# Kernel tuning notes

Hardware: AMD Instinct MI355X
Metric: run time of the kernel (lower is better)

The kernel has to match this reference:

```python
import jax, jax.numpy as jnp
import numpy as np

E, D, O, G, H, K = 8, 1024, 1024, 512, 2048, 2
B = 8192

def _xavier(key, shape):
    fan_in, fan_out = shape[-2], shape[-1]
    lim = float(np.sqrt(6.0 / (fan_in + fan_out)))
    return jax.random.uniform(key, shape, jnp.float32, -lim, lim)

def setup_inputs() -> dict:
    key = jax.random.key(0)
    ks = jax.random.split(key, 6)
    x = jax.random.normal(ks[0], (B, D), jnp.float32)
    # stacked expert params (xavier-uniform weights, zero bias like torch init)
    W1 = _xavier(ks[1], (E, D, H))
    b1 = jnp.zeros((E, H), jnp.float32)
    W2 = _xavier(ks[2], (E, H, O))
    b2 = jnp.zeros((E, O), jnp.float32)
    # gate params
    Wg1 = _xavier(ks[3], (D, G))
    bg1 = jnp.zeros((G,), jnp.float32)
    Wg2 = _xavier(ks[4], (G, E))
    bg2 = jnp.zeros((E,), jnp.float32)
    return {"x": x, "W1": W1, "b1": b1, "W2": W2, "b2": b2,
            "Wg1": Wg1, "bg1": bg1, "Wg2": Wg2, "bg2": bg2}

def reference(x, W1, b1, W2, b2, Wg1, bg1, Wg2, bg2):
    batch = x.shape[0]
    # gate (dropout inactive in eval)
    gate_logits = jax.nn.relu(x @ Wg1 + bg1) @ Wg2 + bg2          # [B,E]
    gate_scores = jax.nn.softmax(gate_logits, axis=1)
    top_k_scores, top_k_indices = jax.lax.top_k(gate_scores, K)   # [B,K]
    # dense all-expert MLP (mirrors torch.stack over experts)
    h = jax.nn.relu(jnp.einsum('bd,edh->ebh', x, W1) + b1[:, None, :])   # [E,B,H]
    expert_outputs = jnp.einsum('ebh,eho->beo', h, W2) + b2[None, :, :]  # [B,E,O]
    # gather top-k expert outputs, scale, combine
    selected = jnp.take_along_axis(expert_outputs, top_k_indices[:, :, None], axis=1)  # [B,K,O]
    scaled = selected * top_k_scores[:, :, None]
    scaled = scaled / (jnp.sum(top_k_scores, axis=1, keepdims=True)[:, :, None] + 1e-9)
    combined = jnp.sum(scaled, axis=1)                            # [B,O]
    # auxiliary loss
    one_hot = jax.nn.one_hot(top_k_indices, E, dtype=jnp.float32) # [B,K,E]
    expert_load = jnp.sum(one_hot, axis=(0, 1)) / (batch + 1e-9)
    load_balancing_loss = jnp.var(expert_load, ddof=1)            # torch var is unbiased
    entropy = -jnp.mean(jnp.sum(gate_scores * jnp.log(gate_scores + 1e-9), axis=1))
    aux_loss = load_balancing_loss + entropy
    return combined, aux_loss
```

## Files before the change

kernel.cpp:

```cpp
#include <hip/hip_runtime.h>

#define B_ 8192
#define D_ 1024
#define O_ 1024
#define G_ 512
#define H_ 2048
#define E_ 8
#define ROWSP (B_ * 2 + E_ * 128)
#define TAU 0.01f

typedef unsigned short u16;
using f32x4 = __attribute__((ext_vector_type(4))) float;
using s16x8 = __attribute__((ext_vector_type(8))) short;

__device__ __forceinline__ u16 f2bf(float f) {
  union { float f; unsigned u; } v; v.f = f;
  unsigned r = v.u + 0x7FFFu + ((v.u >> 16) & 1u);
  return (u16)(r >> 16);
}
__device__ __forceinline__ float bf2f(u16 h) {
  union { unsigned u; float f; } v; v.u = ((unsigned)h) << 16; return v.f;
}
__device__ __forceinline__ void gload16(const void* g, void* l) {
  __builtin_amdgcn_global_load_lds(
      (const __attribute__((address_space(1))) unsigned int*)g,
      (__attribute__((address_space(3))) unsigned int*)l, 16, 0, 0);
}
__device__ __forceinline__ int xcd_swz(int bid, int nwg) {
  return (bid & 7) * (nwg >> 3) + (bid >> 3);
}
__device__ __forceinline__ int stage_kc(int t) {
  return (((t & 3) ^ ((t >> 3) & 3)) * 8);
}
__device__ __forceinline__ int frag_idx(int half, int lane, int i) {
  int row = half * 64 + i * 16 + (lane & 15);
  int s = (lane >> 4) ^ ((lane >> 1) & 3);
  return (row * 4 + s) * 8;
}

#define PREP_CAST_BLK (B_ * D_ / 4 / 256)
#define PREP_WG1_BLK  ((G_ / 32) * (D_ / 32))
#define PREP_W1_BLK   ((H_ / 32) * (D_ / 32) * E_)
#define PREP_W2_BLK   ((O_ / 32) * (H_ / 32) * E_)

__device__ __forceinline__ void tr_cast_tile(const float* __restrict__ src,
                                             u16* __restrict__ dhi,
                                             u16* __restrict__ dlo,
                                             int R, int C, int bx, int by,
                                             float (*tile)[33], int t) {
  int tx = t & 31, ty = t >> 5;
  int c0 = bx * 32, r0 = by * 32;
#pragma unroll
  for (int p = 0; p < 4; ++p) {
    int r = ty + p * 8;
    tile[r][tx] = src[(size_t)(r0 + r) * C + c0 + tx];
  }
  __syncthreads();
#pragma unroll
  for (int p = 0; p < 4; ++p) {
    int r = ty + p * 8;
    float v = tile[tx][r];
    size_t o = (size_t)(c0 + r) * R + r0 + tx;
    dhi[o] = f2bf(v);
    if (dlo) dlo[o] = f2bf(v - bf2f(f2bf(v)));
  }
}

__global__ __launch_bounds__(256) void k_prep(const float* __restrict__ x,
                                              u16* __restrict__ xhi, u16* __restrict__ xlo,
                                              const float* __restrict__ Wg1,
                                              u16* __restrict__ wg1h, u16* __restrict__ wg1l,
                                              const float* __restrict__ W1, u16* __restrict__ w1t,
                                              const float* __restrict__ W2, u16* __restrict__ w2t) {
  __shared__ float tile[32][33];
  int t = threadIdx.x;
  int b = blockIdx.x;
  if (b < PREP_CAST_BLK) {
    int i = b * 256 + t;
    float4 v = ((const float4*)x)[i];
    u16 h0 = f2bf(v.x), h1 = f2bf(v.y), h2 = f2bf(v.z), h3 = f2bf(v.w);
    ushort4 hi; hi.x = h0; hi.y = h1; hi.z = h2; hi.w = h3;
    ushort4 lo;
    lo.x = f2bf(v.x - bf2f(h0)); lo.y = f2bf(v.y - bf2f(h1));
    lo.z = f2bf(v.z - bf2f(h2)); lo.w = f2bf(v.w - bf2f(h3));
    ((ushort4*)xhi)[i] = hi; ((ushort4*)xlo)[i] = lo;
    return;
  }
  b -= PREP_CAST_BLK;
  if (b < PREP_WG1_BLK) {
    tr_cast_tile(Wg1, wg1h, wg1l, D_, G_, b & 15, b >> 4, tile, t);
    return;
  }
  b -= PREP_WG1_BLK;
  if (b < PREP_W1_BLK) {
    int e = b >> 11, rr = b & 2047;
    size_t ofs = (size_t)e * D_ * H_;
    tr_cast_tile(W1 + ofs, w1t + ofs, nullptr, D_, H_, rr & 63, rr >> 6, tile, t);
    return;
  }
  b -= PREP_W1_BLK;
  {
    int e = b >> 11, rr = b & 2047;
    size_t ofs = (size_t)e * H_ * O_;
    tr_cast_tile(W2 + ofs, w2t + ofs, nullptr, H_, O_, rr & 31, rr >> 5, tile, t);
  }
}

__global__ __launch_bounds__(256) void k_gate_gemm1(const u16* __restrict__ xhi,
                                                    const u16* __restrict__ xlo,
                                                    const u16* __restrict__ whi,
                                                    const u16* __restrict__ wlo,
                                                    const float* __restrict__ bg1,
                                                    float* __restrict__ G1) {
  __shared__ u16 Ah[4096], Al[4096], Bh[4096], Bl[4096];
  int work = xcd_swz(blockIdx.x, (G_ / 128) * (B_ / 128));
  int m0 = (work >> 2) * 128, n0 = (work & 3) * 128;
  int t = threadIdx.x;
  int wave = t >> 6, lane = t & 63;
  int wm = wave >> 1, wn = wave & 1;

  const f32x4 z = {0.f, 0.f, 0.f, 0.f};
  f32x4 acc[4][4];
#pragma unroll
  for (int i = 0; i < 4; ++i)
#pragma unroll
    for (int j = 0; j < 4; ++j) acc[i][j] = z;

  int ar = t >> 2, ac = stage_kc(t);
  const u16* xh0 = xhi + (size_t)(m0 + ar) * D_ + ac;
  const u16* xh1 = xhi + (size_t)(m0 + 64 + ar) * D_ + ac;
  const u16* xl0 = xlo + (size_t)(m0 + ar) * D_ + ac;
  const u16* xl1 = xlo + (size_t)(m0 + 64 + ar) * D_ + ac;
  const u16* wh0 = whi + (size_t)(n0 + ar) * D_ + ac;
  const u16* wh1 = whi + (size_t)(n0 + 64 + ar) * D_ + ac;
  const u16* wl0 = wlo + (size_t)(n0 + ar) * D_ + ac;
  const u16* wl1 = wlo + (size_t)(n0 + 64 + ar) * D_ + ac;

  for (int k0 = 0; k0 < D_; k0 += 32) {
    gload16(xh0 + k0, &Ah[t * 8]); gload16(xh1 + k0, &Ah[2048 + t * 8]);
    gload16(xl0 + k0, &Al[t * 8]); gload16(xl1 + k0, &Al[2048 + t * 8]);
    gload16(wh0 + k0, &Bh[t * 8]); gload16(wh1 + k0, &Bh[2048 + t * 8]);
    gload16(wl0 + k0, &Bl[t * 8]); gload16(wl1 + k0, &Bl[2048 + t * 8]);
    __syncthreads();
    s16x8 ah[4], al[4], bh[4], bl[4];
#pragma unroll
    for (int i = 0; i < 4; ++i) {
      ah[i] = *(const s16x8*)&Ah[frag_idx(wm, lane, i)];
      al[i] = *(const s16x8*)&Al[frag_idx(wm, lane, i)];
      bh[i] = *(const s16x8*)&Bh[frag_idx(wn, lane, i)];
      bl[i] = *(const s16x8*)&Bl[frag_idx(wn, lane, i)];
    }
#pragma unroll
    for (int i = 0; i < 4; ++i)
#pragma unroll
      for (int j = 0; j < 4; ++j) {
        acc[i][j] = __builtin_amdgcn_mfma_f32_16x16x32_bf16(ah[i], bh[j], acc[i][j], 0, 0, 0);
        acc[i][j] = __builtin_amdgcn_mfma_f32_16x16x32_bf16(ah[i], bl[j], acc[i][j], 0, 0, 0);
        acc[i][j] = __builtin_amdgcn_mfma_f32_16x16x32_bf16(al[i], bh[j], acc[i][j], 0, 0, 0);
      }
    __syncthreads();
  }
#pragma unroll
  for (int j = 0; j < 4; ++j) {
    int col = n0 + wn * 64 + j * 16 + (lane & 15);
    float bias = bg1[col];
#pragma unroll
    for (int i = 0; i < 4; ++i)
#pragma unroll
      for (int q = 0; q < 4; ++q) {
        int row = m0 + wm * 64 + i * 16 + (lane >> 4) * 4 + q;
        float v = acc[i][j][q] + bias;
        G1[(size_t)row * G_ + col] = v > 0.f ? v : 0.f;
      }
  }
}

__global__ __launch_bounds__(256) void k_gate_logits(const float* __restrict__ G1,
                                                     const float* __restrict__ Wg2,
                                                     const float* __restrict__ bg2,
                                                     float* __restrict__ logits,
                                                     int* __restrict__ flaglist,
                                                     int* __restrict__ nflag) {
  int t = threadIdx.x, wave = t >> 6, lane = t & 63;
  int row = blockIdx.x * 4 + wave;

  float4 g0 = *(const float4*)(G1 + (size_t)row * G_ + lane * 8);
  float4 g1 = *(const float4*)(G1 + (size_t)row * G_ + lane * 8 + 4);
  float g[8] = {g0.x, g0.y, g0.z, g0.w, g1.x, g1.y, g1.z, g1.w};
  float p[8] = {0, 0, 0, 0, 0, 0, 0, 0};
#pragma unroll
  for (int cc = 0; cc < 8; ++cc) {
    int c = lane * 8 + cc;
    float4 w0 = *(const float4*)(Wg2 + c * 8);
    float4 w1 = *(const float4*)(Wg2 + c * 8 + 4);
    p[0] += g[cc] * w0.x; p[1] += g[cc] * w0.y; p[2] += g[cc] * w0.z; p[3] += g[cc] * w0.w;
    p[4] += g[cc] * w1.x; p[5] += g[cc] * w1.y; p[6] += g[cc] * w1.z; p[7] += g[cc] * w1.w;
  }
#pragma unroll
  for (int off = 32; off >= 1; off >>= 1)
#pragma unroll
    for (int e = 0; e < 8; ++e) p[e] += __shfl_xor(p[e], off);
  if (lane == 0) {
    float l1 = -1e30f, l2 = -1e30f, l3 = -1e30f;
#pragma unroll
    for (int e = 0; e < 8; ++e) {
      float v = p[e] + bg2[e];
      logits[(size_t)row * 8 + e] = v;
      if (v > l1) { l3 = l2; l2 = l1; l1 = v; }
      else if (v > l2) { l3 = l2; l2 = v; }
      else if (v > l3) { l3 = v; }
    }
    if (l2 - l3 < TAU) {
      int pos = atomicAdd(nflag, 1);
      flaglist[pos] = row;
    }
  }
}

__global__ __launch_bounds__(256) void k_gate_fixup(const float* __restrict__ x,
                                                    const float* __restrict__ Wg1,
                                                    const float* __restrict__ bg1,
                                                    const float* __restrict__ Wg2,
                                                    const float* __restrict__ bg2,
                                                    const int* __restrict__ flaglist,
                                                    const int* __restrict__ nflag,
                                                    float* __restrict__ logits) {
  __shared__ float xs[1024];
  __shared__ float red[256][9];
  int t = threadIdx.x;
  int n = *nflag;
  for (int i = blockIdx.x; i < n; i += gridDim.x) {
    int row = flaglist[i];
    ((float4*)xs)[t] = ((const float4*)(x + (size_t)row * D_))[t];
    __syncthreads();
    int c0 = t * 2;
    float h0 = 0.f, h1 = 0.f;
#pragma unroll 8
    for (int d = 0; d < D_; ++d) {
      float xv = xs[d];
      float2 w = *(const float2*)(Wg1 + (size_t)d * G_ + c0);
      h0 += xv * w.x; h1 += xv * w.y;
    }
    h0 += bg1[c0]; h1 += bg1[c0 + 1];
    h0 = h0 > 0.f ? h0 : 0.f; h1 = h1 > 0.f ? h1 : 0.f;
#pragma unroll
    for (int e = 0; e < 8; ++e)
      red[t][e] = h0 * Wg2[c0 * 8 + e] + h1 * Wg2[(c0 + 1) * 8 + e];
    __syncthreads();
    for (int s = 128; s >= 1; s >>= 1) {
      if (t < s) {
#pragma unroll
        for (int e = 0; e < 8; ++e) red[t][e] += red[t + s][e];
      }
      __syncthreads();
    }
    if (t < 8) logits[(size_t)row * 8 + t] = red[0][t] + bg2[t];
    __syncthreads();
  }
}

__global__ __launch_bounds__(256) void k_gate_final(const float* __restrict__ logits,
                                                    int* __restrict__ topidx,
                                                    float* __restrict__ wnorm,
                                                    int* __restrict__ counts,
                                                    float* __restrict__ entacc) {
  __shared__ int cnt_s[8];
  __shared__ float ent_s[4];
  int t = threadIdx.x;
  if (t < 8) cnt_s[t] = 0;
  __syncthreads();
  int row = blockIdx.x * 256 + t;
  float4 a = ((const float4*)logits)[(size_t)row * 2];
  float4 b = ((const float4*)logits)[(size_t)row * 2 + 1];
  float L[8] = {a.x, a.y, a.z, a.w, b.x, b.y, b.z, b.w};
  float m = L[0];
#pragma unroll
  for (int e = 1; e < 8; ++e) m = fmaxf(m, L[e]);
  float s[8], Z = 0.f;
#pragma unroll
  for (int e = 0; e < 8; ++e) { s[e] = expf(L[e] - m); Z += s[e]; }
  float inv = 1.f / Z;
  float sc[8];
#pragma unroll
  for (int e = 0; e < 8; ++e) sc[e] = s[e] * inv;
  int i1 = 0;
#pragma unroll
  for (int e = 1; e < 8; ++e) if (L[e] > L[i1]) i1 = e;
  int i2 = (i1 == 0) ? 1 : 0;
#pragma unroll
  for (int e = 0; e < 8; ++e) if (e != i1 && L[e] > L[i2]) i2 = e;
  float s1 = sc[i1], s2 = sc[i2];
  float denom = s1 + s2 + 1e-9f;
  topidx[row * 2] = i1; topidx[row * 2 + 1] = i2;
  wnorm[row * 2] = s1 / denom; wnorm[row * 2 + 1] = s2 / denom;
  atomicAdd(&cnt_s[i1], 1); atomicAdd(&cnt_s[i2], 1);
  float ent = 0.f;
#pragma unroll
  for (int e = 0; e < 8; ++e) ent -= sc[e] * logf(sc[e] + 1e-9f);
#pragma unroll
  for (int off = 32; off >= 1; off >>= 1) ent += __shfl_xor(ent, off);
  if ((t & 63) == 0) ent_s[t >> 6] = ent;
  __syncthreads();
  if (t == 0) atomicAdd(entacc, ent_s[0] + ent_s[1] + ent_s[2] + ent_s[3]);
  if (t < 8) atomicAdd(&counts[t], cnt_s[t]);
}

__global__ void k_scan(const int* __restrict__ counts, const float* __restrict__ entacc,
                       int* __restrict__ aoff, float* __restrict__ aux_out) {
  if (threadIdx.x == 0 && blockIdx.x == 0) {
    int off = 0; aoff[0] = 0;
    float ld[8]; float mean = 0.f;
    for (int e = 0; e < 8; ++e) {
      ld[e] = (float)counts[e] / (8192.0f + 1e-9f);
      mean += ld[e];
      off += ((counts[e] + 127) >> 7) << 7;
      aoff[e + 1] = off;
    }
    mean *= 0.125f;
    float var = 0.f;
    for (int e = 0; e < 8; ++e) { float d = ld[e] - mean; var += d * d; }
    var *= (1.0f / 7.0f);
    *aux_out = var + entacc[0] / 8192.0f;
  }
}

__global__ __launch_bounds__(256) void k_scatter(const int* __restrict__ topidx,
                                                 const float* __restrict__ wnorm,
                                                 const int* __restrict__ aoff,
                                                 int* __restrict__ fill,
                                                 int* __restrict__ tok_list,
                                                 float* __restrict__ wroute,
                                                 int* __restrict__ pos_of) {
  int t = blockIdx.x * 256 + threadIdx.x;
  if (t >= B_ * 2) return;
  int e = topidx[t];
  int pos = aoff[e] + atomicAdd(&fill[e], 1);
  tok_list[pos] = t >> 1;
  wroute[pos] = wnorm[t];
  pos_of[t] = pos;
}

__global__ __launch_bounds__(256) void k_egemm1(const u16* __restrict__ xhi,
                                                const u16* __restrict__ w1t,
                                                const float* __restrict__ b1v,
                                                const int* __restrict__ tok_list,
                                                const int* __restrict__ aoff,
                                                u16* __restrict__ hbuf) {
  __shared__ u16 As[2][8192], Bs[2][8192];
  int work = xcd_swz(blockIdx.x, (H_ / 128) * (ROWSP / 128));
  int rt = work >> 4;
  int n0 = (work & 15) * 128;
  int row0 = rt * 128;
  if (row0 >= aoff[8]) return;
  int e = 0;
  while (row0 >= aoff[e + 1]) ++e;
  int t = threadIdx.x, wave = t >> 6, lane = t & 63;
  int wm = wave >> 1, wn = wave & 1;
  const u16* w1e = w1t + (size_t)e * H_ * D_;

  int ar = t >> 2, ac = stage_kc(t);
  int tok0 = tok_list[row0 + ar];       if ((unsigned)tok0 >= B_) tok0 = 0;
  int tok1 = tok_list[row0 + 64 + ar];  if ((unsigned)tok1 >= B_) tok1 = 0;
  const u16* a0 = xhi + (size_t)tok0 * D_ + ac;
  const u16* a1 = xhi + (size_t)tok1 * D_ + ac;
  const u16* bb0 = w1e + (size_t)(n0 + ar) * D_ + ac;
  const u16* bb1 = w1e + (size_t)(n0 + 64 + ar) * D_ + ac;

  const f32x4 z = {0.f, 0.f, 0.f, 0.f};
  f32x4 acc[4][4];
#pragma unroll
  for (int i = 0; i < 4; ++i)
#pragma unroll
    for (int j = 0; j < 4; ++j) acc[i][j] = z;

#pragma unroll
  for (int s = 0; s < 2; ++s) {
    int kk = s * 32;
    gload16(a0 + kk, &As[0][s * 4096 + t * 8]);
    gload16(a1 + kk, &As[0][s * 4096 + 2048 + t * 8]);
    gload16(bb0 + kk, &Bs[0][s * 4096 + t * 8]);
    gload16(bb1 + kk, &Bs[0][s * 4096 + 2048 + t * 8]);
  }
  __syncthreads();

  const int NT = D_ / 64;
  for (int kt = 0; kt < NT; ++kt) {
    int cur = kt & 1, nxt = cur ^ 1;
    if (kt + 1 < NT) {
      int kb = (kt + 1) * 64;
#pragma unroll
      for (int s = 0; s < 2; ++s) {
        int kk = kb + s * 32;
        gload16(a0 + kk, &As[nxt][s * 4096 + t * 8]);
        gload16(a1 + kk, &As[nxt][s * 4096 + 2048 + t * 8]);
        gload16(bb0 + kk, &Bs[nxt][s * 4096 + t * 8]);
        gload16(bb1 + kk, &Bs[nxt][s * 4096 + 2048 + t * 8]);
      }
    }
#pragma unroll
    for (int s = 0; s < 2; ++s) {
      const u16* Sa = &As[cur][s * 4096];
      const u16* Sb = &Bs[cur][s * 4096];
      s16x8 af[4], bf[4];
#pragma unroll
      for (int i = 0; i < 4; ++i) {
        af[i] = *(const s16x8*)&Sa[frag_idx(wm, lane, i)];
        bf[i] = *(const s16x8*)&Sb[frag_idx(wn, lane, i)];
      }
#pragma unroll
      for (int i = 0; i < 4; ++i)
#pragma unroll
        for (int j = 0; j < 4; ++j)
          acc[i][j] = __builtin_amdgcn_mfma_f32_16x16x32_bf16(af[i], bf[j], acc[i][j], 0, 0, 0);
    }
    __syncthreads();
  }
#pragma unroll
  for (int j = 0; j < 4; ++j) {
    int col = n0 + wn * 64 + j * 16 + (lane & 15);
    float bias = b1v[e * H_ + col];
#pragma unroll
    for (int i = 0; i < 4; ++i)
#pragma unroll
      for (int q = 0; q < 4; ++q) {
        int row = row0 + wm * 64 + i * 16 + (lane >> 4) * 4 + q;
        float v = acc[i][j][q] + bias;
        hbuf[(size_t)row * H_ + col] = f2bf(v > 0.f ? v : 0.f);
      }
  }
}

__global__ __launch_bounds__(256) void k_egemm2(const u16* __restrict__ hbuf,
                                                const u16* __restrict__ w2t,
                                                const float* __restrict__ b2v,
                                                const int* __restrict__ aoff,
                                                const float* __restrict__ wroute,
                                                u16* __restrict__ rbuf) {
  __shared__ u16 As[2][8192], Bs[2][8192];
  int work = xcd_swz(blockIdx.x, (O_ / 128) * (ROWSP / 128));
  int rt = work >> 3;
  int n0 = (work & 7) * 128;
  int row0 = rt * 128;
  if (row0 >= aoff[8]) return;
  int e = 0;
  while (row0 >= aoff[e + 1]) ++e;
  int t = threadIdx.x, wave = t >> 6, lane = t & 63;
  int wm = wave >> 1, wn = wave & 1;
  const u16* w2e = w2t + (size_t)e * O_ * H_;

  int ar = t >> 2, ac = stage_kc(t);
  const u16* a0 = hbuf + (size_t)(row0 + ar) * H_ + ac;
  const u16* a1 = hbuf + (size_t)(row0 + 64 + ar) * H_ + ac;
  const u16* bb0 = w2e + (size_t)(n0 + ar) * H_ + ac;
  const u16* bb1 = w2e + (size_t)(n0 + 64 + ar) * H_ + ac;

  const f32x4 z = {0.f, 0.f, 0.f, 0.f};
  f32x4 acc[4][4];
#pragma unroll
  for (int i = 0; i < 4; ++i)
#pragma unroll
    for (int j = 0; j < 4; ++j) acc[i][j] = z;

#pragma unroll
  for (int s = 0; s < 2; ++s) {
    int kk = s * 32;
    gload16(a0 + kk, &As[0][s * 4096 + t * 8]);
    gload16(a1 + kk, &As[0][s * 4096 + 2048 + t * 8]);
    gload16(bb0 + kk, &Bs[0][s * 4096 + t * 8]);
    gload16(bb1 + kk, &Bs[0][s * 4096 + 2048 + t * 8]);
  }
  __syncthreads();

  const int NT = H_ / 64;
  for (int kt = 0; kt < NT; ++kt) {
    int cur = kt & 1, nxt = cur ^ 1;
    if (kt + 1 < NT) {
      int kb = (kt + 1) * 64;
#pragma unroll
      for (int s = 0; s < 2; ++s) {
        int kk = kb + s * 32;
        gload16(a0 + kk, &As[nxt][s * 4096 + t * 8]);
        gload16(a1 + kk, &As[nxt][s * 4096 + 2048 + t * 8]);
        gload16(bb0 + kk, &Bs[nxt][s * 4096 + t * 8]);
        gload16(bb1 + kk, &Bs[nxt][s * 4096 + 2048 + t * 8]);
      }
    }
#pragma unroll
    for (int s = 0; s < 2; ++s) {
      const u16* Sa = &As[cur][s * 4096];
      const u16* Sb = &Bs[cur][s * 4096];
      s16x8 af[4], bf[4];
#pragma unroll
      for (int i = 0; i < 4; ++i) {
        af[i] = *(const s16x8*)&Sa[frag_idx(wm, lane, i)];
        bf[i] = *(const s16x8*)&Sb[frag_idx(wn, lane, i)];
      }
#pragma unroll
      for (int i = 0; i < 4; ++i)
#pragma unroll
        for (int j = 0; j < 4; ++j)
          acc[i][j] = __builtin_amdgcn_mfma_f32_16x16x32_bf16(af[i], bf[j], acc[i][j], 0, 0, 0);
    }
    __syncthreads();
  }
#pragma unroll
  for (int i = 0; i < 4; ++i)
#pragma unroll
    for (int q = 0; q < 4; ++q) {
      int row = row0 + wm * 64 + i * 16 + (lane >> 4) * 4 + q;
      float wv = wroute[row];
#pragma unroll
      for (int j = 0; j < 4; ++j) {
        int col = n0 + wn * 64 + j * 16 + (lane & 15);
        float bias = b2v[e * O_ + col];
        rbuf[(size_t)row * O_ + col] = f2bf((acc[i][j][q] + bias) * wv);
      }
    }
}

__global__ __launch_bounds__(256) void k_combine(const u16* __restrict__ rbuf,
                                                 const int* __restrict__ pos_of,
                                                 float* __restrict__ out) {
  int t = threadIdx.x;
  int tok = blockIdx.x * 2 + (t >> 7);
  int c = (t & 127) * 8;
  int p0 = pos_of[tok * 2], p1 = pos_of[tok * 2 + 1];
  const u16* r0 = rbuf + (size_t)p0 * O_ + c;
  const u16* r1 = rbuf + (size_t)p1 * O_ + c;
  ushort4 a0 = *(const ushort4*)r0, a1 = *(const ushort4*)(r0 + 4);
  ushort4 b0 = *(const ushort4*)r1, b1 = *(const ushort4*)(r1 + 4);
  float4 o0, o1;
  o0.x = bf2f(a0.x) + bf2f(b0.x); o0.y = bf2f(a0.y) + bf2f(b0.y);
  o0.z = bf2f(a0.z) + bf2f(b0.z); o0.w = bf2f(a0.w) + bf2f(b0.w);
  o1.x = bf2f(a1.x) + bf2f(b1.x); o1.y = bf2f(a1.y) + bf2f(b1.y);
  o1.z = bf2f(a1.z) + bf2f(b1.z); o1.w = bf2f(a1.w) + bf2f(b1.w);
  float* op = out + (size_t)tok * O_ + c;
  *(float4*)op = o0; *(float4*)(op + 4) = o1;
}

static const size_t o_xhi  = 0;
static const size_t o_xlo  = o_xhi + (size_t)B_ * D_ * 2;
static const size_t o_w1t  = o_xlo + (size_t)B_ * D_ * 2;
static const size_t o_w2t  = o_w1t + (size_t)E_ * H_ * D_ * 2;
static const size_t o_wg1h = o_w2t + (size_t)E_ * O_ * H_ * 2;
static const size_t o_wg1l = o_wg1h + (size_t)G_ * D_ * 2;
static const size_t o_G1   = o_wg1l + (size_t)G_ * D_ * 2;
static const size_t o_h    = o_G1 + (size_t)B_ * G_ * 4;
static const size_t o_idx  = o_h + (size_t)ROWSP * H_ * 2;
static const size_t o_wn   = o_idx + (size_t)B_ * 2 * 4;
static const size_t o_pos  = o_wn + (size_t)B_ * 2 * 4;
static const size_t o_tok  = o_pos + (size_t)B_ * 2 * 4;
static const size_t o_wr   = o_tok + (size_t)ROWSP * 4;
static const size_t o_cnt  = o_wr + (size_t)ROWSP * 4;
static const size_t o_fill = o_cnt + 32;
static const size_t o_ent  = o_cnt + 64;
static const size_t o_nfl  = o_cnt + 96;
static const size_t o_aoff = o_cnt + 128;
static const size_t o_logits = o_cnt + 256;
static const size_t o_flag   = o_logits + (size_t)B_ * 8 * 4;
static const size_t o_rbuf = o_xlo;

extern "C" void kernel_launch(void* const* d_in, const int* in_sizes, int n_in,
                              void* d_out, int out_size, void* d_ws, size_t ws_size,
                              hipStream_t stream) {
  const float* x   = (const float*)d_in[0];
  const float* W1  = (const float*)d_in[1];
  const float* b1  = (const float*)d_in[2];
  const float* W2  = (const float*)d_in[3];
  const float* b2  = (const float*)d_in[4];
  const float* Wg1 = (const float*)d_in[5];
  const float* bg1 = (const float*)d_in[6];
  const float* Wg2 = (const float*)d_in[7];
  const float* bg2 = (const float*)d_in[8];
  float* out = (float*)d_out;
  char* ws = (char*)d_ws;

  u16* xhi  = (u16*)(ws + o_xhi);
  u16* xlo  = (u16*)(ws + o_xlo);
  u16* w1t  = (u16*)(ws + o_w1t);
  u16* w2t  = (u16*)(ws + o_w2t);
  u16* wg1h = (u16*)(ws + o_wg1h);
  u16* wg1l = (u16*)(ws + o_wg1l);
  float* G1 = (float*)(ws + o_G1);
  u16* hbuf = (u16*)(ws + o_h);
  int* topidx = (int*)(ws + o_idx);
  float* wnorm = (float*)(ws + o_wn);
  int* pos_of = (int*)(ws + o_pos);
  int* tok_list = (int*)(ws + o_tok);
  float* wroute = (float*)(ws + o_wr);
  int* counts = (int*)(ws + o_cnt);
  int* fill = (int*)(ws + o_fill);
  float* entacc = (float*)(ws + o_ent);
  int* nflag = (int*)(ws + o_nfl);
  int* aoff = (int*)(ws + o_aoff);
  float* logits = (float*)(ws + o_logits);
  int* flaglist = (int*)(ws + o_flag);
  u16* rbuf = (u16*)(ws + o_rbuf);

  hipMemsetAsync(ws + o_cnt, 0, 128, stream);

  k_prep<<<PREP_CAST_BLK + PREP_WG1_BLK + PREP_W1_BLK + PREP_W2_BLK, 256, 0, stream>>>(
      x, xhi, xlo, Wg1, wg1h, wg1l, W1, w1t, W2, w2t);

  k_gate_gemm1<<<(G_ / 128) * (B_ / 128), 256, 0, stream>>>(xhi, xlo, wg1h, wg1l, bg1, G1);
  k_gate_logits<<<B_ / 4, 256, 0, stream>>>(G1, Wg2, bg2, logits, flaglist, nflag);
  k_gate_fixup<<<128, 256, 0, stream>>>(x, Wg1, bg1, Wg2, bg2, flaglist, nflag, logits);
  k_gate_final<<<B_ / 256, 256, 0, stream>>>(logits, topidx, wnorm, counts, entacc);
  k_scan<<<1, 64, 0, stream>>>(counts, entacc, aoff, out + (size_t)B_ * O_);
  k_scatter<<<(B_ * 2) / 256, 256, 0, stream>>>(topidx, wnorm, aoff, fill, tok_list, wroute, pos_of);

  k_egemm1<<<(H_ / 128) * (ROWSP / 128), 256, 0, stream>>>(xhi, w1t, b1, tok_list, aoff, hbuf);
  k_egemm2<<<(O_ / 128) * (ROWSP / 128), 256, 0, stream>>>(hbuf, w2t, b2, aoff, wroute, rbuf);
  k_combine<<<B_ / 2, 256, 0, stream>>>(rbuf, pos_of, out);
}
```

Baseline: 559.3 us.

## Use 256x256 tiles with 8 waves and phased MFMA/load interleaving in expert GEMMs

Both expert GEMMs switch from 128x128 tiles with 4 waves to 256x256 tiles with 8 waves (512 threads). Each wave now accumulates a 128x64 sub-tile. The K loop becomes a hand-scheduled four-phase loop: LDS fragment reads, async global-to-LDS prefetches and MFMA bursts are interleaved, with explicit s_waitcnt, barriers and s_setprio to keep the matrix units busy and raise arithmetic intensity per byte loaded. Expert row padding grows to multiples of 256 so row tiles do not cross experts. This wastes more padded rows, reduces the number of workgroups and raises register pressure, and the hand-written waitcnt/barrier choreography is fragile.

```diff
diff --git a/kernel.cpp b/kernel.cpp
--- a/kernel.cpp
+++ b/kernel.cpp
@@ -6,7 +6,7 @@
 #define G_ 512
 #define H_ 2048
 #define E_ 8
-#define ROWSP (B_ * 2 + E_ * 128)
+#define ROWSP (B_ * 2 + E_ * 256)
 #define TAU 0.01f
 
 typedef unsigned short u16;
@@ -37,6 +37,10 @@
   int s = (lane >> 4) ^ ((lane >> 1) & 3);
   return (row * 4 + s) * 8;
 }
+
+#define VMW(N) asm volatile("s_waitcnt vmcnt(" #N ")" ::: "memory")
+#define LGKM0  asm volatile("s_waitcnt lgkmcnt(0)" ::: "memory")
+#define MF(M, N, A, Bv) acc[M][N] = __builtin_amdgcn_mfma_f32_16x16x32_bf16(A, Bv, acc[M][N], 0, 0, 0)
 
 #define PREP_CAST_BLK (B_ * D_ / 4 / 256)
 #define PREP_WG1_BLK  ((G_ / 32) * (D_ / 32))
@@ -313,7 +317,7 @@
     for (int e = 0; e < 8; ++e) {
       ld[e] = (float)counts[e] / (8192.0f + 1e-9f);
       mean += ld[e];
-      off += ((counts[e] + 127) >> 7) << 7;
+      off += ((counts[e] + 255) >> 8) << 8;
       aoff[e + 1] = off;
     }
     mean *= 0.125f;
@@ -340,180 +344,152 @@
   pos_of[t] = pos;
 }
 
-__global__ __launch_bounds__(256) void k_egemm1(const u16* __restrict__ xhi,
-                                                const u16* __restrict__ w1t,
-                                                const float* __restrict__ b1v,
-                                                const int* __restrict__ tok_list,
-                                                const int* __restrict__ aoff,
-                                                u16* __restrict__ hbuf) {
-  __shared__ u16 As[2][8192], Bs[2][8192];
-  int work = xcd_swz(blockIdx.x, (H_ / 128) * (ROWSP / 128));
-  int rt = work >> 4;
-  int n0 = (work & 15) * 128;
-  int row0 = rt * 128;
+
+#define EG_PH(MFMAS)                                   \
+  __builtin_amdgcn_s_barrier();                        \
+  LGKM0;                                               \
+  __builtin_amdgcn_s_setprio(1);                       \
+  MFMAS;                                               \
+  __builtin_amdgcn_s_setprio(0);                       \
+  __builtin_amdgcn_s_barrier();
+
+#define EG_KLOOP(NT, KDIM)                                                          \
+  gload16(gA0, As + t * 8);                                      \
+  gload16(gA1, As + 4096 + t * 8);                                       \
+  gload16(gB0, Bs + t * 8);                                              \
+  gload16(gB1, Bs + 4096 + t * 8);                                       \
+  gload16(gB0 + 32, Bs + 2 * 4096 + t * 8);                      \
+  gload16(gB1 + 32, Bs + 3 * 4096 + t * 8);                              \
+  VMW(2);                                                                           \
+  __builtin_amdgcn_s_barrier();                                                     \
+  for (int kt = 0; kt < (NT); ++kt) {                                               \
+    int buf = kt & 1;                                                               \
+    const u16* SA = As + (buf * 2 + wm) * 4096;                                     \
+    const u16* SB = Bs + (buf * 2 + (wn >> 1)) * 4096;                              \
+    s16x8 a0, a1, a2, a3, b0, b1, b2, b3;                                           \
+                                              \
+    a0 = *(const s16x8*)&SA[frag_idx(0, lane, 0)];                                  \
+    a1 = *(const s16x8*)&SA[frag_idx(0, lane, 1)];                                  \
+    a2 = *(const s16x8*)&SA[frag_idx(0, lane, 2)];                                  \
+    a3 = *(const s16x8*)&SA[frag_idx(0, lane, 3)];                                  \
+    b0 = *(const s16x8*)&SB[frag_idx(wn & 1, lane, 0)];                             \
+    b1 = *(const s16x8*)&SB[frag_idx(wn & 1, lane, 1)];                             \
+    if (kt + 1 < (NT)) gload16(gA0 + (kt + 1) * 32, As + ((buf ^ 1) * 2) * 4096 + t * 8); \
+    EG_PH(MF(0,0,a0,b0); MF(1,0,a1,b0); MF(2,0,a2,b0); MF(3,0,a3,b0);               \
+          MF(0,1,a0,b1); MF(1,1,a1,b1); MF(2,1,a2,b1); MF(3,1,a3,b1);)              \
+                                                               \
+    b2 = *(const s16x8*)&SB[frag_idx(wn & 1, lane, 2)];                             \
+    b3 = *(const s16x8*)&SB[frag_idx(wn & 1, lane, 3)];                             \
+    if (kt + 1 < (NT)) gload16(gA1 + (kt + 1) * 32, As + ((buf ^ 1) * 2 + 1) * 4096 + t * 8); \
+    EG_PH(MF(0,2,a0,b2); MF(1,2,a1,b2); MF(2,2,a2,b2); MF(3,2,a3,b2);               \
+          MF(0,3,a0,b3); MF(1,3,a1,b3); MF(2,3,a2,b3); MF(3,3,a3,b3);)              \
+                                                       \
+    a0 = *(const s16x8*)&SA[frag_idx(1, lane, 0)];                                  \
+    a1 = *(const s16x8*)&SA[frag_idx(1, lane, 1)];                                  \
+    a2 = *(const s16x8*)&SA[frag_idx(1, lane, 2)];                                  \
+    a3 = *(const s16x8*)&SA[frag_idx(1, lane, 3)];                                  \
+    if (kt + 2 < (NT)) gload16(gB0 + (kt + 2) * 32, Bs + (buf * 2) * 4096 + t * 8); \
+    EG_PH(MF(4,2,a0,b2); MF(5,2,a1,b2); MF(6,2,a2,b2); MF(7,2,a3,b2);               \
+          MF(4,3,a0,b3); MF(5,3,a1,b3); MF(6,3,a2,b3); MF(7,3,a3,b3);)              \
+                                                                       \
+    if (kt + 2 < (NT)) gload16(gB1 + (kt + 2) * 32, Bs + (buf * 2 + 1) * 4096 + t * 8); \
+    if (kt < (NT) - 2) { VMW(2); } else { VMW(0); }                                 \
+    EG_PH(MF(4,0,a0,b0); MF(5,0,a1,b0); MF(6,0,a2,b0); MF(7,0,a3,b0);               \
+          MF(4,1,a0,b1); MF(5,1,a1,b1); MF(6,1,a2,b1); MF(7,1,a3,b1);)              \
+  }
+
+__global__ __launch_bounds__(512, 2) void k_egemm1(const u16* __restrict__ xhi,
+                                                   const u16* __restrict__ w1t,
+                                                   const float* __restrict__ b1v,
+                                                   const int* __restrict__ tok_list,
+                                                   const int* __restrict__ aoff,
+                                                   u16* __restrict__ hbuf) {
+  __shared__ u16 As[4 * 4096], Bs[4 * 4096];
+  int work = xcd_swz(blockIdx.x, (ROWSP / 256) * (H_ / 256));
+  int rt = work >> 3, n0 = (work & 7) * 256;
+  int row0 = rt * 256;
   if (row0 >= aoff[8]) return;
   int e = 0;
   while (row0 >= aoff[e + 1]) ++e;
-  int t = threadIdx.x, wave = t >> 6, lane = t & 63;
-  int wm = wave >> 1, wn = wave & 1;
+  int t = threadIdx.x, lane = t & 63, wave = t >> 6;
+  int wm = wave >> 2, wn = wave & 3;
   const u16* w1e = w1t + (size_t)e * H_ * D_;
 
   int ar = t >> 2, ac = stage_kc(t);
-  int tok0 = tok_list[row0 + ar];       if ((unsigned)tok0 >= B_) tok0 = 0;
-  int tok1 = tok_list[row0 + 64 + ar];  if ((unsigned)tok1 >= B_) tok1 = 0;
-  const u16* a0 = xhi + (size_t)tok0 * D_ + ac;
-  const u16* a1 = xhi + (size_t)tok1 * D_ + ac;
-  const u16* bb0 = w1e + (size_t)(n0 + ar) * D_ + ac;
-  const u16* bb1 = w1e + (size_t)(n0 + 64 + ar) * D_ + ac;
-
+  int tok0 = tok_list[row0 + ar];        if ((unsigned)tok0 >= B_) tok0 = 0;
+  int tok1 = tok_list[row0 + 128 + ar];  if ((unsigned)tok1 >= B_) tok1 = 0;
+  const u16* gA0 = xhi + (size_t)tok0 * D_ + ac;
+  const u16* gA1 = xhi + (size_t)tok1 * D_ + ac;
+  const u16* gB0 = w1e + (size_t)(n0 + ar) * D_ + ac;
+  const u16* gB1 = w1e + (size_t)(n0 + 128 + ar) * D_ + ac;
+
+  f32x4 acc[8][4];
   const f32x4 z = {0.f, 0.f, 0.f, 0.f};
-  f32x4 acc[4][4];
-#pragma unroll
-  for (int i = 0; i < 4; ++i)
+#pragma unroll
+  for (int i = 0; i < 8; ++i)
 #pragma unroll
     for (int j = 0; j < 4; ++j) acc[i][j] = z;
 
-#pragma unroll
-  for (int s = 0; s < 2; ++s) {
-    int kk = s * 32;
-    gload16(a0 + kk, &As[0][s * 4096 + t * 8]);
-    gload16(a1 + kk, &As[0][s * 4096 + 2048 + t * 8]);
-    gload16(bb0 + kk, &Bs[0][s * 4096 + t * 8]);
-    gload16(bb1 + kk, &Bs[0][s * 4096 + 2048 + t * 8]);
-  }
-  __syncthreads();
-
-  const int NT = D_ / 64;
-  for (int kt = 0; kt < NT; ++kt) {
-    int cur = kt & 1, nxt = cur ^ 1;
-    if (kt + 1 < NT) {
-      int kb = (kt + 1) * 64;
-#pragma unroll
-      for (int s = 0; s < 2; ++s) {
-        int kk = kb + s * 32;
-        gload16(a0 + kk, &As[nxt][s * 4096 + t * 8]);
-        gload16(a1 + kk, &As[nxt][s * 4096 + 2048 + t * 8]);
-        gload16(bb0 + kk, &Bs[nxt][s * 4096 + t * 8]);
-        gload16(bb1 + kk, &Bs[nxt][s * 4096 + 2048 + t * 8]);
-      }
-    }
-#pragma unroll
-    for (int s = 0; s < 2; ++s) {
-      const u16* Sa = &As[cur][s * 4096];
-      const u16* Sb = &Bs[cur][s * 4096];
-      s16x8 af[4], bf[4];
-#pragma unroll
-      for (int i = 0; i < 4; ++i) {
-        af[i] = *(const s16x8*)&Sa[frag_idx(wm, lane, i)];
-        bf[i] = *(const s16x8*)&Sb[frag_idx(wn, lane, i)];
-      }
-#pragma unroll
-      for (int i = 0; i < 4; ++i)
-#pragma unroll
-        for (int j = 0; j < 4; ++j)
-          acc[i][j] = __builtin_amdgcn_mfma_f32_16x16x32_bf16(af[i], bf[j], acc[i][j], 0, 0, 0);
-    }
-    __syncthreads();
-  }
-#pragma unroll
-  for (int j = 0; j < 4; ++j) {
-    int col = n0 + wn * 64 + j * 16 + (lane & 15);
+  EG_KLOOP(D_ / 32, D_)
+
+#pragma unroll
+  for (int n = 0; n < 4; ++n) {
+    int col = n0 + wn * 64 + n * 16 + (lane & 15);
     float bias = b1v[e * H_ + col];
 #pragma unroll
-    for (int i = 0; i < 4; ++i)
+    for (int m = 0; m < 8; ++m)
 #pragma unroll
       for (int q = 0; q < 4; ++q) {
-        int row = row0 + wm * 64 + i * 16 + (lane >> 4) * 4 + q;
-        float v = acc[i][j][q] + bias;
+        int row = row0 + wm * 128 + m * 16 + (lane >> 4) * 4 + q;
+        float v = acc[m][n][q] + bias;
         hbuf[(size_t)row * H_ + col] = f2bf(v > 0.f ? v : 0.f);
       }
   }
 }
 
-__global__ __launch_bounds__(256) void k_egemm2(const u16* __restrict__ hbuf,
-                                                const u16* __restrict__ w2t,
-                                                const float* __restrict__ b2v,
-                                                const int* __restrict__ aoff,
-                                                const float* __restrict__ wroute,
-                                                u16* __restrict__ rbuf) {
-  __shared__ u16 As[2][8192], Bs[2][8192];
-  int work = xcd_swz(blockIdx.x, (O_ / 128) * (ROWSP / 128));
-  int rt = work >> 3;
-  int n0 = (work & 7) * 128;
-  int row0 = rt * 128;
+__global__ __launch_bounds__(512, 2) void k_egemm2(const u16* __restrict__ hbuf,
+                                                   const u16* __restrict__ w2t,
+                                                   const float* __restrict__ b2v,
+                                                   const int* __restrict__ aoff,
+                                                   const float* __restrict__ wroute,
+                                                   u16* __restrict__ rbuf) {
+  __shared__ u16 As[4 * 4096], Bs[4 * 4096];
+  int work = xcd_swz(blockIdx.x, (ROWSP / 256) * (O_ / 256));
+  int rt = work >> 2, n0 = (work & 3) * 256;
+  int row0 = rt * 256;
   if (row0 >= aoff[8]) return;
   int e = 0;
   while (row0 >= aoff[e + 1]) ++e;
-  int t = threadIdx.x, wave = t >> 6, lane = t & 63;
-  int wm = wave >> 1, wn = wave & 1;
+  int t = threadIdx.x, lane = t & 63, wave = t >> 6;
+  int wm = wave >> 2, wn = wave & 3;
   const u16* w2e = w2t + (size_t)e * O_ * H_;
 
   int ar = t >> 2, ac = stage_kc(t);
-  const u16* a0 = hbuf + (size_t)(row0 + ar) * H_ + ac;
-  const u16* a1 = hbuf + (size_t)(row0 + 64 + ar) * H_ + ac;
-  const u16* bb0 = w2e + (size_t)(n0 + ar) * H_ + ac;
-  const u16* bb1 = w2e + (size_t)(n0 + 64 + ar) * H_ + ac;
-
+  const u16* gA0 = hbuf + (size_t)(row0 + ar) * H_ + ac;
+  const u16* gA1 = hbuf + (size_t)(row0 + 128 + ar) * H_ + ac;
+  const u16* gB0 = w2e + (size_t)(n0 + ar) * H_ + ac;
+  const u16* gB1 = w2e + (size_t)(n0 + 128 + ar) * H_ + ac;
+
+  f32x4 acc[8][4];
   const f32x4 z = {0.f, 0.f, 0.f, 0.f};
-  f32x4 acc[4][4];
-#pragma unroll
-  for (int i = 0; i < 4; ++i)
+#pragma unroll
+  for (int i = 0; i < 8; ++i)
 #pragma unroll
     for (int j = 0; j < 4; ++j) acc[i][j] = z;
 
-#pragma unroll
-  for (int s = 0; s < 2; ++s) {
-    int kk = s * 32;
-    gload16(a0 + kk, &As[0][s * 4096 + t * 8]);
-    gload16(a1 + kk, &As[0][s * 4096 + 2048 + t * 8]);
-    gload16(bb0 + kk, &Bs[0][s * 4096 + t * 8]);
-    gload16(bb1 + kk, &Bs[0][s * 4096 + 2048 + t * 8]);
-  }
-  __syncthreads();
-
-  const int NT = H_ / 64;
-  for (int kt = 0; kt < NT; ++kt) {
-    int cur = kt & 1, nxt = cur ^ 1;
-    if (kt + 1 < NT) {
-      int kb = (kt + 1) * 64;
-#pragma unroll
-      for (int s = 0; s < 2; ++s) {
-        int kk = kb + s * 32;
-        gload16(a0 + kk, &As[nxt][s * 4096 + t * 8]);
-        gload16(a1 + kk, &As[nxt][s * 4096 + 2048 + t * 8]);
-        gload16(bb0 + kk, &Bs[nxt][s * 4096 + t * 8]);
-        gload16(bb1 + kk, &Bs[nxt][s * 4096 + 2048 + t * 8]);
-      }
-    }
-#pragma unroll
-    for (int s = 0; s < 2; ++s) {
-      const u16* Sa = &As[cur][s * 4096];
-      const u16* Sb = &Bs[cur][s * 4096];
-      s16x8 af[4], bf[4];
-#pragma unroll
-      for (int i = 0; i < 4; ++i) {
-        af[i] = *(const s16x8*)&Sa[frag_idx(wm, lane, i)];
-        bf[i] = *(const s16x8*)&Sb[frag_idx(wn, lane, i)];
-      }
-#pragma unroll
-      for (int i = 0; i < 4; ++i)
-#pragma unroll
-        for (int j = 0; j < 4; ++j)
-          acc[i][j] = __builtin_amdgcn_mfma_f32_16x16x32_bf16(af[i], bf[j], acc[i][j], 0, 0, 0);
-    }
-    __syncthreads();
-  }
-#pragma unroll
-  for (int i = 0; i < 4; ++i)
+  EG_KLOOP(H_ / 32, H_)
+
+#pragma unroll
+  for (int m = 0; m < 8; ++m)
 #pragma unroll
     for (int q = 0; q < 4; ++q) {
-      int row = row0 + wm * 64 + i * 16 + (lane >> 4) * 4 + q;
+      int row = row0 + wm * 128 + m * 16 + (lane >> 4) * 4 + q;
       float wv = wroute[row];
 #pragma unroll
-      for (int j = 0; j < 4; ++j) {
-        int col = n0 + wn * 64 + j * 16 + (lane & 15);
+      for (int n = 0; n < 4; ++n) {
+        int col = n0 + wn * 64 + n * 16 + (lane & 15);
         float bias = b2v[e * O_ + col];
-        rbuf[(size_t)row * O_ + col] = f2bf((acc[i][j][q] + bias) * wv);
+        rbuf[(size_t)row * O_ + col] = f2bf((acc[m][n][q] + bias) * wv);
       }
     }
 }
@@ -609,7 +585,7 @@
   k_scan<<<1, 64, 0, stream>>>(counts, entacc, aoff, out + (size_t)B_ * O_);
   k_scatter<<<(B_ * 2) / 256, 256, 0, stream>>>(topidx, wnorm, aoff, fill, tok_list, wroute, pos_of);
 
-  k_egemm1<<<(H_ / 128) * (ROWSP / 128), 256, 0, stream>>>(xhi, w1t, b1, tok_list, aoff, hbuf);
-  k_egemm2<<<(O_ / 128) * (ROWSP / 128), 256, 0, stream>>>(hbuf, w2t, b2, aoff, wroute, rbuf);
+  k_egemm1<<<(ROWSP / 256) * (H_ / 256), 512, 0, stream>>>(xhi, w1t, b1, tok_list, aoff, hbuf);
+  k_egemm2<<<(ROWSP / 256) * (O_ / 256), 512, 0, stream>>>(hbuf, w2t, b2, aoff, wroute, rbuf);
   k_combine<<<B_ / 2, 256, 0, stream>>>(rbuf, pos_of, out);
 }
```

Result: slower. 579.9 us (+3.7%).
